# Kernel optimization log

Measured on AMD Instinct MI355X. Metric: run time of the kernel, lower is better.

## Reference

```python
import jax, jax.numpy as jnp
import numpy as np
from jax import lax

DECAY = 0.99
EPS = 1e-5


def setup_inputs() -> dict:
    key = jax.random.key(0)
    k1, k2, k3 = jax.random.split(key, 3)
    x = jax.random.normal(k1, (32, 64, 64, 64), dtype=jnp.float32)  # NCHW, C == embedding_dim
    embedding = jax.random.normal(k2, (512, 64), dtype=jnp.float32)  # [K, D] codebook
    cluster_size = jnp.ones((512,), dtype=jnp.float32)  # EMA buffer
    embedding_avg = jax.random.normal(k3, (512, 64), dtype=jnp.float32)  # EMA buffer
    return {"x": x, "embedding": embedding, "cluster_size": cluster_size, "embedding_avg": embedding_avg}


def reference(x, embedding, cluster_size, embedding_avg):
    n, c, h, w = x.shape
    K, D = embedding.shape
    # [N, D] flattened tokens (NHWC order, matching permute(0,2,3,1))
    flat_x = jnp.transpose(x, (0, 2, 3, 1)).reshape(-1, D)
    distances = (
        jnp.sum(flat_x ** 2, axis=1, keepdims=True)
        + jnp.sum(embedding ** 2, axis=1)
        - 2.0 * flat_x @ embedding.T
    )  # [N, K]
    idxs = jnp.argmin(distances, axis=1)  # [N]
    # one_hot @ embedding == gather (same math, no [N,K] one-hot GEMM)
    quantized = embedding[idxs].reshape(n, h, w, c)
    quantized = jnp.transpose(quantized, (0, 3, 1, 2))  # back to NCHW
    loss = jnp.mean((x - lax.stop_gradient(quantized)) ** 2)
    # EMA updates (training path). segment_sum == one_hot.sum(0) / flat_x.T @ one_hot
    ones = jnp.ones((flat_x.shape[0],), dtype=x.dtype)
    batch_cluster_size = jax.ops.segment_sum(ones, idxs, num_segments=K)  # [K]
    batch_embedding_avg = jax.ops.segment_sum(flat_x, idxs, num_segments=K)  # [K, D]
    new_cluster_size = cluster_size * DECAY + (1.0 - DECAY) * batch_cluster_size
    new_embedding_avg = embedding_avg * DECAY + (1.0 - DECAY) * batch_embedding_avg
    new_embedding = new_embedding_avg / (new_cluster_size + EPS)[:, None]
    # straight-through estimator
    quantized_st = x + lax.stop_gradient(quantized - x)
    return quantized_st, loss, new_embedding, new_cluster_size, new_embedding_avg
```

## Files before the change

### kernel.cpp

```cpp
#include <hip/hip_runtime.h>

#define HW 4096
#define KC 512

typedef __attribute__((ext_vector_type(8))) short s16x8;
typedef __attribute__((ext_vector_type(16))) float f32x16;

__device__ inline short f2bf(float f) {
    unsigned int u = __builtin_bit_cast(unsigned int, f);
    unsigned int lsb = (u >> 16) & 1u;
    u += 0x7fffu + lsb;
    return (short)(u >> 16);
}
__device__ inline float bf2f(short h) {
    unsigned int u = ((unsigned int)(unsigned short)h) << 16;
    return __builtin_bit_cast(float, u);
}

#define WS_EN    133136
#define WS_EHF   135184
#define WS_ELF   217104
#define WS_IDX   282640

__global__ void k_prep_en(const float* __restrict__ emb, float* __restrict__ en) {
    int m = blockIdx.x * 256 + threadIdx.x;
    if (m >= KC) return;
    const float* e = emb + m * 64;
    float d0 = 0.f, d1 = 0.f, d2 = 0.f, d3 = 0.f;
#pragma unroll
    for (int c = 0; c < 64; c += 4) {
        d0 = fmaf(e[c], e[c], d0);
        d1 = fmaf(e[c + 1], e[c + 1], d1);
        d2 = fmaf(e[c + 2], e[c + 2], d2);
        d3 = fmaf(e[c + 3], e[c + 3], d3);
    }
    en[m] = (d0 + d1) + (d2 + d3);
}

__global__ void k_prep_frag(const float* __restrict__ emb, const float* __restrict__ en,
                            short* __restrict__ ehf, short* __restrict__ elf) {
    int t = blockIdx.x * 256 + threadIdx.x;
    int m = t >> 3, ko = t & 7;
    int mt = m >> 5, ks = ko >> 1;
    int lane = (m & 31) + 32 * (ko & 1);
    s16x8 hv, lv;
#pragma unroll
    for (int j = 0; j < 8; ++j) {
        float v = emb[m * 64 + ko * 8 + j];
        short h = f2bf(v);
        hv[j] = h;
        lv[j] = f2bf(v - bf2f(h));
    }
    ((s16x8*)ehf)[(mt * 5 + ks) * 64 + lane] = hv;
    ((s16x8*)elf)[(mt * 4 + ks) * 64 + lane] = lv;

    int e2 = t * 2;
    int mt2 = e2 >> 9;
    int lane2 = (e2 >> 3) & 63;
    int j2 = e2 & 7;
    unsigned int val = 0;
    if (lane2 < 32 && j2 == 0) {
        float ev = en[mt2 * 32 + (lane2 & 31)];
        short eh_ = f2bf(ev);
        short el_ = f2bf(ev - bf2f(eh_));
        val = ((unsigned int)(unsigned short)eh_) | (((unsigned int)(unsigned short)el_) << 16);
    }
    *(unsigned int*)(ehf + ((size_t)(mt2 * 5 + 4) * 64 + lane2) * 8 + j2) = val;
}

__device__ inline void merge2(float& s1, int& i1, float& s2, int& i2,
                              float os1, int oi1, float os2, int oi2) {
    bool ob = (os1 < s1) || (os1 == s1 && oi1 < i1);
    float n1s = ob ? os1 : s1;  int n1i = ob ? oi1 : i1;
    float ls  = ob ? s1  : os1; int li  = ob ? i1  : oi1;
    float ws  = ob ? os2 : s2;  int wi  = ob ? oi2 : i2;
    bool b2 = (ls < ws) || (ls == ws && li < wi);
    s1 = n1s; i1 = n1i;
    s2 = b2 ? ls : ws; i2 = b2 ? li : wi;
}

__global__ __launch_bounds__(512, 2) void k_main(const float* __restrict__ x,
                                              const short* __restrict__ ehf,
                                              const short* __restrict__ elf,
                                              const float* __restrict__ en,
                                              const float* __restrict__ emb,
                                              float* __restrict__ qout,
                                              unsigned short* __restrict__ idx_out,
                                              float* __restrict__ loss_acc) {
    __shared__ short shH[16 * 5 * 64 * 8];
    __shared__ short shL[16 * 4 * 64 * 8];

    int tid = threadIdx.x;
    int wv = tid >> 6, lane = tid & 63;
    int tb = blockIdx.x * 512;
    int n = tb >> 12, hwb = tb & 4095;
    const float* xp = x + (size_t)n * 64 * HW;
    int wbase = hwb + wv * 64;

    {
        const s16x8* ehg = (const s16x8*)ehf;
        const s16x8* elg = (const s16x8*)elf;
        s16x8* sH = (s16x8*)shH;
        s16x8* sL = (s16x8*)shL;
#pragma unroll
        for (int i = 0; i < 10; ++i) sH[i * 512 + tid] = ehg[i * 512 + tid];
#pragma unroll
        for (int i = 0; i < 8; ++i) sL[i * 512 + tid] = elg[i * 512 + tid];
    }

    int l5 = lane & 31;
    int kh = (lane >> 5) * 8;

    s16x8 fah[5], fbh[5], fal[4], fbl[4];
    {
        const float* pa = xp + wbase + l5;
        const float* pb = pa + 32;
#pragma unroll
        for (int ks = 0; ks < 4; ++ks) {
            s16x8 ha, la, hb, lb;
#pragma unroll
            for (int j = 0; j < 8; ++j) {
                int c = ks * 16 + kh + j;
                float va = -2.0f * pa[(size_t)c * HW];
                float vb = -2.0f * pb[(size_t)c * HW];
                short h0 = f2bf(va); ha[j] = h0; la[j] = f2bf(va - bf2f(h0));
                short h1 = f2bf(vb); hb[j] = h1; lb[j] = f2bf(vb - bf2f(h1));
            }
            fah[ks] = ha; fal[ks] = la; fbh[ks] = hb; fbl[ks] = lb;
        }
        s16x8 v0;
#pragma unroll
        for (int j = 0; j < 8; ++j) v0[j] = 0;
        if (lane < 32) { v0[0] = (short)0x3F80; v0[1] = (short)0x3F80; }
        fah[4] = v0; fbh[4] = v0;
    }

    __syncthreads();

    const s16x8* sH8 = (const s16x8*)shH;
    const s16x8* sL8 = (const s16x8*)shL;

    float s1a = 3.402823466e38f, s2a = 3.402823466e38f;
    float s1b = 3.402823466e38f, s2b = 3.402823466e38f;
    int i1a = 0, i2a = 0, i1b = 0, i2b = 0;
    int hv4 = (lane >> 5) * 4;

#pragma unroll 2
    for (int mt = 0; mt < 16; ++mt) {
        s16x8 ah[5], al[4];
#pragma unroll
        for (int ks = 0; ks < 5; ++ks) ah[ks] = sH8[(mt * 5 + ks) * 64 + lane];
#pragma unroll
        for (int ks = 0; ks < 4; ++ks) al[ks] = sL8[(mt * 4 + ks) * 64 + lane];

        f32x16 acc0, acc1;
#pragma unroll
        for (int r = 0; r < 16; ++r) { acc0[r] = 0.0f; acc1[r] = 0.0f; }
#pragma unroll
        for (int ks = 0; ks < 5; ++ks) {
            acc0 = __builtin_amdgcn_mfma_f32_32x32x16_bf16(ah[ks], fah[ks], acc0, 0, 0, 0);
            acc1 = __builtin_amdgcn_mfma_f32_32x32x16_bf16(ah[ks], fbh[ks], acc1, 0, 0, 0);
        }
#pragma unroll
        for (int ks = 0; ks < 4; ++ks) {
            acc0 = __builtin_amdgcn_mfma_f32_32x32x16_bf16(al[ks], fah[ks], acc0, 0, 0, 0);
            acc1 = __builtin_amdgcn_mfma_f32_32x32x16_bf16(al[ks], fbh[ks], acc1, 0, 0, 0);
        }
#pragma unroll
        for (int ks = 0; ks < 4; ++ks) {
            acc0 = __builtin_amdgcn_mfma_f32_32x32x16_bf16(ah[ks], fal[ks], acc0, 0, 0, 0);
            acc1 = __builtin_amdgcn_mfma_f32_32x32x16_bf16(ah[ks], fbl[ks], acc1, 0, 0, 0);
        }

        int mb = mt * 32 + hv4;
#pragma unroll
        for (int r = 0; r < 16; ++r) {
            int mi = mb + (r & 3) + 8 * (r >> 2);
            {
                float s = acc0[r];
                bool c1 = s < s1a, c2 = s < s2a;
                s2a = c1 ? s1a : (c2 ? s : s2a); i2a = c1 ? i1a : (c2 ? mi : i2a);
                s1a = c1 ? s : s1a;              i1a = c1 ? mi : i1a;
            }
            {
                float s = acc1[r];
                bool c1 = s < s1b, c2 = s < s2b;
                s2b = c1 ? s1b : (c2 ? s : s2b); i2b = c1 ? i1b : (c2 ? mi : i2b);
                s1b = c1 ? s : s1b;              i1b = c1 ? mi : i1b;
            }
        }
    }

    merge2(s1a, i1a, s2a, i2a, __shfl_xor(s1a, 32), __shfl_xor(i1a, 32),
           __shfl_xor(s2a, 32), __shfl_xor(i2a, 32));
    merge2(s1b, i1b, s2b, i2b, __shfl_xor(s1b, 32), __shfl_xor(i1b, 32),
           __shfl_xor(s2b, 32), __shfl_xor(i2b, 32));

    bool hi = (lane & 32) != 0;
    int I1 = hi ? i1b : i1a;
    int I2 = hi ? i2b : i2a;

    int hw = wbase + lane;
    const float* xq = xp + hw;
    float xv[64];
#pragma unroll
    for (int c = 0; c < 64; ++c) xv[c] = xq[(size_t)c * HW];

    float sxx;
    {
        float d0 = 0.f, d1 = 0.f, d2 = 0.f, d3 = 0.f;
#pragma unroll
        for (int c = 0; c < 64; c += 4) {
            d0 = fmaf(xv[c], xv[c], d0);
            d1 = fmaf(xv[c + 1], xv[c + 1], d1);
            d2 = fmaf(xv[c + 2], xv[c + 2], d2);
            d3 = fmaf(xv[c + 3], xv[c + 3], d3);
        }
        sxx = (d0 + d1) + (d2 + d3);
    }

    int ia = (I1 < I2) ? I1 : I2;
    int ib = (I1 < I2) ? I2 : I1;
    float sa, sb;
    {
        const float4* er = (const float4*)(emb + (size_t)ia * 64);
        float d0 = 0.f, d1 = 0.f, d2 = 0.f, d3 = 0.f;
#pragma unroll
        for (int q = 0; q < 16; ++q) {
            float4 e4 = er[q];
            d0 = fmaf(xv[q * 4], e4.x, d0);
            d1 = fmaf(xv[q * 4 + 1], e4.y, d1);
            d2 = fmaf(xv[q * 4 + 2], e4.z, d2);
            d3 = fmaf(xv[q * 4 + 3], e4.w, d3);
        }
        sa = (sxx + en[ia]) - 2.0f * ((d0 + d1) + (d2 + d3));
    }
    {
        const float4* er = (const float4*)(emb + (size_t)ib * 64);
        float d0 = 0.f, d1 = 0.f, d2 = 0.f, d3 = 0.f;
#pragma unroll
        for (int q = 0; q < 16; ++q) {
            float4 e4 = er[q];
            d0 = fmaf(xv[q * 4], e4.x, d0);
            d1 = fmaf(xv[q * 4 + 1], e4.y, d1);
            d2 = fmaf(xv[q * 4 + 2], e4.z, d2);
            d3 = fmaf(xv[q * 4 + 3], e4.w, d3);
        }
        sb = (sxx + en[ib]) - 2.0f * ((d0 + d1) + (d2 + d3));
    }
    int win = (sb < sa) ? ib : ia;

    idx_out[tb + wv * 64 + lane] = (unsigned short)win;

    const float4* ew = (const float4*)(emb + (size_t)win * 64);
    float* qp = qout + (size_t)n * 64 * HW + hw;
    float l0 = 0.f, l1 = 0.f, l2 = 0.f, l3 = 0.f;
#pragma unroll
    for (int q = 0; q < 16; ++q) {
        float4 e4 = ew[q];
        qp[(size_t)(q * 4) * HW] = e4.x;
        qp[(size_t)(q * 4 + 1) * HW] = e4.y;
        qp[(size_t)(q * 4 + 2) * HW] = e4.z;
        qp[(size_t)(q * 4 + 3) * HW] = e4.w;
        float f0 = xv[q * 4] - e4.x, f1 = xv[q * 4 + 1] - e4.y;
        float f2 = xv[q * 4 + 2] - e4.z, f3 = xv[q * 4 + 3] - e4.w;
        l0 = fmaf(f0, f0, l0);
        l1 = fmaf(f1, f1, l1);
        l2 = fmaf(f2, f2, l2);
        l3 = fmaf(f3, f3, l3);
    }
    float lp = (l0 + l1) + (l2 + l3);
#pragma unroll
    for (int off = 32; off; off >>= 1) lp += __shfl_down(lp, off);
    if (lane == 0) atomicAdd(loss_acc, lp);
}

__global__ __launch_bounds__(1024) void k_seg(const float* __restrict__ x,
                                              const unsigned short* __restrict__ idx,
                                              float* __restrict__ cnt_g,
                                              float* __restrict__ avg_g) {
    __shared__ float acc[KC * 9];
    __shared__ float cnt[KC];
    int tid = threadIdx.x;
    int b = blockIdx.x;
    int n = b >> 4;
    int cg = (b >> 1) & 7;
    int h = b & 1;

    for (int i = tid; i < KC * 9; i += 1024) acc[i] = 0.f;
    if (cg == 0 && tid < KC) cnt[tid] = 0.f;
    __syncthreads();

    const float* xp = x + (size_t)n * 64 * HW + (size_t)(cg * 8) * HW + h * 2048;
    const unsigned short* ip = idx + n * HW + h * 2048;

#pragma unroll
    for (int p = 0; p < 2; ++p) {
        int hw = p * 1024 + tid;
        int k = ip[hw];
        if (cg == 0) atomicAdd(&cnt[k], 1.0f);
        float* row = acc + k * 9;
#pragma unroll
        for (int j = 0; j < 8; ++j) {
            atomicAdd(&row[j], xp[(size_t)j * HW + hw]);
        }
    }
    __syncthreads();

    for (int i = tid; i < KC * 8; i += 1024) {
        int k = i >> 3, j = i & 7;
        atomicAdd(&avg_g[k * 64 + cg * 8 + j], acc[k * 9 + j]);
    }
    if (cg == 0 && tid < KC) atomicAdd(&cnt_g[tid], cnt[tid]);
}

__global__ void k_fin(const float* __restrict__ cs_in, const float* __restrict__ avg_in,
                      const float* __restrict__ cnt, const float* __restrict__ avgacc,
                      const float* __restrict__ loss_acc,
                      float* __restrict__ loss_out, float* __restrict__ emb_out,
                      float* __restrict__ cs_out, float* __restrict__ avg_out) {
    int i = blockIdx.x * 256 + threadIdx.x;
    if (i >= KC * 64) return;
    int k = i >> 6, c = i & 63;
    float ncs = cs_in[k] * 0.99f + 0.01f * cnt[k];
    float nav = avg_in[i] * 0.99f + 0.01f * avgacc[i];
    avg_out[i] = nav;
    emb_out[i] = nav / (ncs + 1e-5f);
    if (c == 0) cs_out[k] = ncs;
    if (i == 0) loss_out[0] = loss_acc[0] * (1.0f / 8388608.0f);
}

extern "C" void kernel_launch(void* const* d_in, const int* in_sizes, int n_in,
                              void* d_out, int out_size, void* d_ws, size_t ws_size,
                              hipStream_t stream) {
    (void)in_sizes; (void)n_in; (void)out_size; (void)ws_size;
    const float* x   = (const float*)d_in[0];
    const float* emb = (const float*)d_in[1];
    const float* cs  = (const float*)d_in[2];
    const float* avg = (const float*)d_in[3];

    float* out      = (float*)d_out;
    float* qout     = out;
    float* loss_out = out + 8388608;
    float* emb_out  = loss_out + 1;
    float* cs_out   = emb_out + 32768;
    float* avg_out  = cs_out + 512;

    char* wsb = (char*)d_ws;
    float* cnt_acc  = (float*)wsb;
    float* avg_acc  = (float*)(wsb + 2048);
    float* loss_acc = (float*)(wsb + 133120);
    float* en       = (float*)(wsb + WS_EN);
    short* ehf      = (short*)(wsb + WS_EHF);
    short* elf      = (short*)(wsb + WS_ELF);
    unsigned short* idx = (unsigned short*)(wsb + WS_IDX);

    hipMemsetAsync(d_ws, 0, 133124, stream);
    k_prep_en<<<2, 256, 0, stream>>>(emb, en);
    k_prep_frag<<<16, 256, 0, stream>>>(emb, en, ehf, elf);
    k_main<<<256, 512, 0, stream>>>(x, ehf, elf, en, emb, qout, idx, loss_acc);
    k_seg<<<512, 1024, 0, stream>>>(x, idx, cnt_acc, avg_acc);
    k_fin<<<128, 256, 0, stream>>>(cs, avg, cnt_acc, avg_acc, loss_acc,
                                   loss_out, emb_out, cs_out, avg_out);
}
```

Baseline: 139.5 us.

## Stage fp32 codebook in LDS for rescoring; read bf16 MFMA operands from global

The shared-memory buffer that held the bf16 hi/lo codebook split for the MFMA distance loop is replaced by a padded fp32 copy of the codebook plus its norms (66 floats per row). The MFMA loop now reads its A operands directly from global memory (L2/L1-resident), while the exact fp32 rescoring of the top-2 candidates and the quantized-output gather read rows from LDS instead of doing random global gathers. This trades cached global loads in the hot MFMA loop for cheaper scattered reads in the epilogue. LDS use rises to about 135 KB per block, which may limit the two-blocks-per-CU occupancy the launch bounds target.

```diff
diff --git a/kernel.cpp b/kernel.cpp
--- a/kernel.cpp
+++ b/kernel.cpp
@@ -87,8 +87,7 @@
                                               float* __restrict__ qout,
                                               unsigned short* __restrict__ idx_out,
                                               float* __restrict__ loss_acc) {
-    __shared__ short shH[16 * 5 * 64 * 8];
-    __shared__ short shL[16 * 4 * 64 * 8];
+    __shared__ float se[KC * 66];
 
     int tid = threadIdx.x;
     int wv = tid >> 6, lane = tid & 63;
@@ -98,14 +97,15 @@
     int wbase = hwb + wv * 64;
 
     {
-        const s16x8* ehg = (const s16x8*)ehf;
-        const s16x8* elg = (const s16x8*)elf;
-        s16x8* sH = (s16x8*)shH;
-        s16x8* sL = (s16x8*)shL;
-#pragma unroll
-        for (int i = 0; i < 10; ++i) sH[i * 512 + tid] = ehg[i * 512 + tid];
-#pragma unroll
-        for (int i = 0; i < 8; ++i) sL[i * 512 + tid] = elg[i * 512 + tid];
+        const float2* eg = (const float2*)emb;
+#pragma unroll
+        for (int i = 0; i < 32; ++i) {
+            int id2 = i * 512 + tid;
+            int row = id2 >> 5, h = id2 & 31;
+            float2 v = eg[id2];
+            *(float2*)&se[row * 66 + h * 2] = v;
+        }
+        se[tid * 66 + 64] = en[tid];
     }
 
     int l5 = lane & 31;
@@ -137,8 +137,8 @@
 
     __syncthreads();
 
-    const s16x8* sH8 = (const s16x8*)shH;
-    const s16x8* sL8 = (const s16x8*)shL;
+    const s16x8* eh8 = (const s16x8*)ehf;
+    const s16x8* el8 = (const s16x8*)elf;
 
     float s1a = 3.402823466e38f, s2a = 3.402823466e38f;
     float s1b = 3.402823466e38f, s2b = 3.402823466e38f;
@@ -149,9 +149,9 @@
     for (int mt = 0; mt < 16; ++mt) {
         s16x8 ah[5], al[4];
 #pragma unroll
-        for (int ks = 0; ks < 5; ++ks) ah[ks] = sH8[(mt * 5 + ks) * 64 + lane];
-#pragma unroll
-        for (int ks = 0; ks < 4; ++ks) al[ks] = sL8[(mt * 4 + ks) * 64 + lane];
+        for (int ks = 0; ks < 5; ++ks) ah[ks] = eh8[(mt * 5 + ks) * 64 + lane];
+#pragma unroll
+        for (int ks = 0; ks < 4; ++ks) al[ks] = el8[(mt * 4 + ks) * 64 + lane];
 
         f32x16 acc0, acc1;
 #pragma unroll
@@ -221,49 +221,52 @@
 
     int ia = (I1 < I2) ? I1 : I2;
     int ib = (I1 < I2) ? I2 : I1;
+    const float* ra = se + ia * 66;
+    const float* rb = se + ib * 66;
     float sa, sb;
     {
-        const float4* er = (const float4*)(emb + (size_t)ia * 64);
         float d0 = 0.f, d1 = 0.f, d2 = 0.f, d3 = 0.f;
 #pragma unroll
-        for (int q = 0; q < 16; ++q) {
-            float4 e4 = er[q];
-            d0 = fmaf(xv[q * 4], e4.x, d0);
-            d1 = fmaf(xv[q * 4 + 1], e4.y, d1);
-            d2 = fmaf(xv[q * 4 + 2], e4.z, d2);
-            d3 = fmaf(xv[q * 4 + 3], e4.w, d3);
-        }
-        sa = (sxx + en[ia]) - 2.0f * ((d0 + d1) + (d2 + d3));
-    }
-    {
-        const float4* er = (const float4*)(emb + (size_t)ib * 64);
+        for (int c = 0; c < 64; c += 4) {
+            float2 p0 = *(const float2*)&ra[c];
+            float2 p1 = *(const float2*)&ra[c + 2];
+            d0 = fmaf(xv[c], p0.x, d0);
+            d1 = fmaf(xv[c + 1], p0.y, d1);
+            d2 = fmaf(xv[c + 2], p1.x, d2);
+            d3 = fmaf(xv[c + 3], p1.y, d3);
+        }
+        sa = (sxx + ra[64]) - 2.0f * ((d0 + d1) + (d2 + d3));
+    }
+    {
         float d0 = 0.f, d1 = 0.f, d2 = 0.f, d3 = 0.f;
 #pragma unroll
-        for (int q = 0; q < 16; ++q) {
-            float4 e4 = er[q];
-            d0 = fmaf(xv[q * 4], e4.x, d0);
-            d1 = fmaf(xv[q * 4 + 1], e4.y, d1);
-            d2 = fmaf(xv[q * 4 + 2], e4.z, d2);
-            d3 = fmaf(xv[q * 4 + 3], e4.w, d3);
-        }
-        sb = (sxx + en[ib]) - 2.0f * ((d0 + d1) + (d2 + d3));
+        for (int c = 0; c < 64; c += 4) {
+            float2 p0 = *(const float2*)&rb[c];
+            float2 p1 = *(const float2*)&rb[c + 2];
+            d0 = fmaf(xv[c], p0.x, d0);
+            d1 = fmaf(xv[c + 1], p0.y, d1);
+            d2 = fmaf(xv[c + 2], p1.x, d2);
+            d3 = fmaf(xv[c + 3], p1.y, d3);
+        }
+        sb = (sxx + rb[64]) - 2.0f * ((d0 + d1) + (d2 + d3));
     }
     int win = (sb < sa) ? ib : ia;
 
     idx_out[tb + wv * 64 + lane] = (unsigned short)win;
 
-    const float4* ew = (const float4*)(emb + (size_t)win * 64);
+    const float* rw = (win == ia) ? ra : rb;
     float* qp = qout + (size_t)n * 64 * HW + hw;
     float l0 = 0.f, l1 = 0.f, l2 = 0.f, l3 = 0.f;
 #pragma unroll
-    for (int q = 0; q < 16; ++q) {
-        float4 e4 = ew[q];
-        qp[(size_t)(q * 4) * HW] = e4.x;
-        qp[(size_t)(q * 4 + 1) * HW] = e4.y;
-        qp[(size_t)(q * 4 + 2) * HW] = e4.z;
-        qp[(size_t)(q * 4 + 3) * HW] = e4.w;
-        float f0 = xv[q * 4] - e4.x, f1 = xv[q * 4 + 1] - e4.y;
-        float f2 = xv[q * 4 + 2] - e4.z, f3 = xv[q * 4 + 3] - e4.w;
+    for (int c = 0; c < 64; c += 4) {
+        float2 p0 = *(const float2*)&rw[c];
+        float2 p1 = *(const float2*)&rw[c + 2];
+        qp[(size_t)c * HW] = p0.x;
+        qp[(size_t)(c + 1) * HW] = p0.y;
+        qp[(size_t)(c + 2) * HW] = p1.x;
+        qp[(size_t)(c + 3) * HW] = p1.y;
+        float f0 = xv[c] - p0.x, f1 = xv[c + 1] - p0.y;
+        float f2 = xv[c + 2] - p1.x, f3 = xv[c + 3] - p1.y;
         l0 = fmaf(f0, f0, l0);
         l1 = fmaf(f1, f1, l1);
         l2 = fmaf(f2, f2, l2);
```

Measured after the change: 135.0 us. 1.03x faster.
